# Kernel tuning notes

Hardware: AMD Instinct MI355X
Metric: run time of the kernel (lower is better)

Reference implementation:

```python
import jax, jax.numpy as jnp
import numpy as np

DIM, DIM_HEAD, S, R = 1024, 64, 8, 2
SCALE = DIM_HEAD ** -0.5
NEG = -jnp.finfo(jnp.float32).max


def setup_inputs() -> dict:
    key = jax.random.key(0)
    ks = jax.random.split(key, 7)
    b, n = 2, 2048
    x = jax.random.normal(ks[0], (b, n, DIM), dtype=jnp.float32)
    mask = jnp.ones((b, n), dtype=bool)
    sd, rd = DIM_HEAD * S, DIM_HEAD * R
    init = lambda k, i, o: jax.random.normal(k, (i, o), dtype=jnp.float32) / np.sqrt(i)
    return {
        'x': x,
        'mask': mask,
        'Wsq': init(ks[1], DIM, sd),
        'Wsk': init(ks[2], DIM, sd),
        'Wrv': init(ks[3], DIM, rd),
        'Wrq': init(ks[4], DIM, sd),
        'Wrk': init(ks[5], DIM_HEAD, DIM_HEAD),
        'Wout': init(ks[6], sd, DIM),
    }


def _split_heads(t, h):
    # b n (h d) -> b h n d
    b, n, hd = t.shape
    return t.reshape(b, n, h, hd // h).transpose(0, 2, 1, 3)


def reference(x, mask, Wsq, Wsk, Wrv, Wrq, Wrk, Wout):
    # --- search stage ---
    sq = _split_heads(x @ Wsq, S) * SCALE          # b s i d
    sk = _split_heads(x @ Wsk, S)                  # b s j d
    search_sim = jnp.einsum('bsid,bsjd->bsij', sq, sk)
    search_sim = jnp.where(mask[:, None, None, :], search_sim, NEG)
    search_attn = jax.nn.softmax(search_sim, axis=-1)
    # --- retrieval stage ---
    rv = _split_heads(x @ Wrv, R)                  # b r j d
    retrieved = jnp.einsum('bsij,brjd->bsrid', search_attn, rv)  # b s r n d
    rq = _split_heads(x @ Wrq, S) * SCALE          # b s n d
    rk = retrieved @ Wrk                           # b s r n d
    retrieval_sim = jnp.einsum('bsnd,bsrnd->bsnr', rq, rk)
    retrieval_attn = jax.nn.softmax(retrieval_sim, axis=-1)
    out = jnp.einsum('bsnr,bsrnd->bsnd', retrieval_attn, retrieved)
    b, _, n, d = out.shape
    out = out.transpose(0, 2, 1, 3).reshape(b, n, S * d)  # b n (s d)
    return out @ Wout
```

## Files before the change

### kernel.cpp

```cpp
#include <hip/hip_runtime.h>

typedef unsigned short u16;
typedef unsigned int u32;
typedef __attribute__((ext_vector_type(8))) short short8;
typedef __attribute__((ext_vector_type(4))) float f32x4;

#define B_     2
#define N_     2048
#define DIMX   1024
#define DH     64
#define NS     8
#define SD     512
#define RD     128

__device__ __forceinline__ float bu2f(u16 u) {
    return __uint_as_float(((unsigned)u) << 16);
}
__device__ __forceinline__ u16 f2bu(float f) {
    unsigned u = __float_as_uint(f);
    return (u16)((u + 0x7FFFu + ((u >> 16) & 1u)) >> 16);
}
__device__ __forceinline__ int swzA(int row, int col) {
    return row * 64 + (col ^ ((row & 7) << 3));
}

__global__ void detect_f32(const u16* __restrict__ wrk, int* __restrict__ flag) {
    __shared__ int cnt;
    if (threadIdx.x == 0) cnt = 0;
    __syncthreads();
    int local = 0;
    for (int k = threadIdx.x; k < 2048; k += 256) {
        u16 u = wrk[2 * k];
        int e = (u >> 7) & 0xFF;
        if (u == 0 || (e >= 0x60 && e <= 0x7E)) local++;
    }
    atomicAdd(&cnt, local);
    __syncthreads();
    if (threadIdx.x == 0) *flag = (cnt < 1024) ? 1 : 0;
}

__global__ __launch_bounds__(256, 4)
void convert_bf16(const void* __restrict__ src, u16* __restrict__ dst, int n8,
                  const int* __restrict__ flag) {
    const bool f32m = (*flag != 0);
    int idx = blockIdx.x * blockDim.x + threadIdx.x;
    int stride = gridDim.x * blockDim.x;
    for (int c = idx; c < n8; c += stride) {
        if (f32m) {
            const float4* s = (const float4*)src;
            float4 v0 = s[c * 2], v1 = s[c * 2 + 1];
            u16 o[8] = {f2bu(v0.x), f2bu(v0.y), f2bu(v0.z), f2bu(v0.w),
                        f2bu(v1.x), f2bu(v1.y), f2bu(v1.z), f2bu(v1.w)};
            *reinterpret_cast<short8*>(&dst[c * 8]) = *reinterpret_cast<short8*>(o);
        } else {
            *reinterpret_cast<short8*>(&dst[c * 8]) =
                reinterpret_cast<const short8*>(src)[c];
        }
    }
}

__global__ __launch_bounds__(256, 4)
void prep_weights(const void* __restrict__ Wsq, const void* __restrict__ Wsk,
                  const void* __restrict__ Wrq, const void* __restrict__ Wrv,
                  const void* __restrict__ Wout, const void* __restrict__ Wrk,
                  u16* __restrict__ wTcat, u16* __restrict__ woutT,
                  u16* __restrict__ wrkb, const int* __restrict__ flag) {
    const bool f32m = (*flag != 0);
    const int b = blockIdx.x, tid = threadIdx.x;

    if (b == 2176) {
#pragma unroll
        for (int t = 0; t < 2; ++t) {
            int c = tid + (t << 8);
            if (f32m) {
                const float4* s = (const float4*)Wrk;
                float4 v0 = s[c * 2], v1 = s[c * 2 + 1];
                u16 o[8] = {f2bu(v0.x), f2bu(v0.y), f2bu(v0.z), f2bu(v0.w),
                            f2bu(v1.x), f2bu(v1.y), f2bu(v1.z), f2bu(v1.w)};
                *reinterpret_cast<short8*>(&wrkb[c * 8]) = *reinterpret_cast<short8*>(o);
            } else {
                *reinterpret_cast<short8*>(&wrkb[c * 8]) =
                    reinterpret_cast<const short8*>(Wrk)[c];
            }
        }
        return;
    }

    const void* W; u16* dst; int K, N, t;
    if (b < 512)        { W = Wsq;  dst = wTcat;               K = DIMX; N = SD;   t = b; }
    else if (b < 1024)  { W = Wsk;  dst = wTcat + 512 * 1024;  K = DIMX; N = SD;   t = b - 512; }
    else if (b < 1536)  { W = Wrq;  dst = wTcat + 1024 * 1024; K = DIMX; N = SD;   t = b - 1024; }
    else if (b < 1664)  { W = Wrv;  dst = wTcat + 1536 * 1024; K = DIMX; N = RD;   t = b - 1536; }
    else                { W = Wout; dst = woutT;               K = SD;   N = DIMX; t = b - 1664; }
    const int ntn = N >> 5;
    const int k0 = (t / ntn) << 5, n0 = (t % ntn) << 5;

    __shared__ float T[32][33];
    const int r = tid >> 3, c4 = (tid & 7) << 2;
    if (f32m) {
        float4 v = *reinterpret_cast<const float4*>(
            &((const float*)W)[(size_t)(k0 + r) * N + n0 + c4]);
        T[r][c4 + 0] = v.x; T[r][c4 + 1] = v.y;
        T[r][c4 + 2] = v.z; T[r][c4 + 3] = v.w;
    } else {
        ushort4 v = *reinterpret_cast<const ushort4*>(
            &((const u16*)W)[(size_t)(k0 + r) * N + n0 + c4]);
        T[r][c4 + 0] = bu2f(v.x); T[r][c4 + 1] = bu2f(v.y);
        T[r][c4 + 2] = bu2f(v.z); T[r][c4 + 3] = bu2f(v.w);
    }
    __syncthreads();
    ushort4 st;
    st.x = f2bu(T[c4 + 0][r]); st.y = f2bu(T[c4 + 1][r]);
    st.z = f2bu(T[c4 + 2][r]); st.w = f2bu(T[c4 + 3][r]);
    *reinterpret_cast<ushort4*>(&dst[(size_t)(n0 + r) * K + k0 + c4]) = st;
}

template <int MODE>
__global__ __launch_bounds__(256, 2)
void gemm_mfma(const u16* __restrict__ A, const u16* __restrict__ Bt,
               void* __restrict__ C0, void* __restrict__ C1,
               void* __restrict__ C2, void* __restrict__ C3,
               int M, int N, int K, const int* __restrict__ flag) {
    __shared__ u16 As[4096];
    __shared__ u16 Bs[8192];
    const int tid = threadIdx.x, lane = tid & 63, w = tid >> 6;
    const int i = lane & 15, g = lane >> 4;
    const int row0 = blockIdx.y << 6, n0 = blockIdx.x << 7;

    f32x4 acc[8];
#pragma unroll
    for (int c = 0; c < 8; ++c) acc[c] = (f32x4){0.f, 0.f, 0.f, 0.f};

    for (int kt = 0; kt < K; kt += 64) {
        __syncthreads();
#pragma unroll
        for (int t2 = 0; t2 < 2; ++t2) {
            int v = tid + (t2 << 8);
            int r = v >> 3, c8 = (v & 7) << 3;
            *reinterpret_cast<short8*>(&As[swzA(r, c8)]) =
                *reinterpret_cast<const short8*>(&A[(size_t)(row0 + r) * K + kt + c8]);
        }
#pragma unroll
        for (int t4 = 0; t4 < 4; ++t4) {
            int v = tid + (t4 << 8);
            int n = v >> 3, c8 = (v & 7) << 3;
            *reinterpret_cast<short8*>(&Bs[swzA(n, c8)]) =
                *reinterpret_cast<const short8*>(&Bt[(size_t)(n0 + n) * K + kt + c8]);
        }
        __syncthreads();
#pragma unroll
        for (int ks = 0; ks < 2; ++ks) {
            short8 a = *reinterpret_cast<const short8*>(&As[swzA(w * 16 + i, ks * 32 + g * 8)]);
#pragma unroll
            for (int cf = 0; cf < 8; ++cf) {
                short8 b = *reinterpret_cast<const short8*>(&Bs[swzA(cf * 16 + i, ks * 32 + g * 8)]);
                acc[cf] = __builtin_amdgcn_mfma_f32_16x16x32_bf16(a, b, acc[cf], 0, 0, 0);
            }
        }
    }

    if (MODE == 0) {
        u16* dst; int ld, off; float alpha;
        if (n0 < 512)       { dst = (u16*)C0; ld = 512; off = n0;        alpha = 0.125f; }
        else if (n0 < 1024) { dst = (u16*)C1; ld = 512; off = n0 - 512;  alpha = 1.f; }
        else if (n0 < 1536) { dst = (u16*)C2; ld = 512; off = n0 - 1024; alpha = 0.125f; }
        else                { dst = (u16*)C3; ld = 128; off = n0 - 1536; alpha = 1.f; }
#pragma unroll
        for (int cf = 0; cf < 8; ++cf)
#pragma unroll
            for (int r = 0; r < 4; ++r)
                dst[(size_t)(row0 + w * 16 + g * 4 + r) * ld + off + cf * 16 + i] =
                    f2bu(acc[cf][r] * alpha);
    } else {
        const bool f32o = (*flag != 0);
        if (f32o) {
            float* Cf = (float*)C0;
#pragma unroll
            for (int cf = 0; cf < 8; ++cf)
#pragma unroll
                for (int r = 0; r < 4; ++r)
                    Cf[(size_t)(row0 + w * 16 + g * 4 + r) * N + n0 + cf * 16 + i] = acc[cf][r];
        } else {
            u16* Cb = (u16*)C0;
#pragma unroll
            for (int cf = 0; cf < 8; ++cf)
#pragma unroll
                for (int r = 0; r < 4; ++r)
                    Cb[(size_t)(row0 + w * 16 + g * 4 + r) * N + n0 + cf * 16 + i] =
                        f2bu(acc[cf][r]);
        }
    }
}

__global__ __launch_bounds__(256, 2)
void flash_mfma(const u16* __restrict__ sq, const u16* __restrict__ sk,
                const u16* __restrict__ rv, const u16* __restrict__ rq,
                const u16* __restrict__ wrk, u16* __restrict__ O) {
    __shared__ u16 Ks[2][64 * 72];
    __shared__ u16 Vt[2][128 * 72];
    __shared__ u16 Ps[4][16 * 72];

    const int tid = threadIdx.x, lane = tid & 63, w = tid >> 6;
    const int i = lane & 15, g = lane >> 4;
    const int bs = blockIdx.y, bi = bs >> 3, si = bs & 7;
    const int q0 = blockIdx.x << 6;

    const u16* sqp = sq + ((size_t)(bi * N_ + q0 + w * 16 + i)) * SD + si * DH;
    const u16* rqp = rq + ((size_t)(bi * N_ + q0 + w * 16 + i)) * SD + si * DH;
    const u16* skb = sk + (size_t)bi * N_ * SD + si * DH;
    const u16* rvb = rv + (size_t)bi * N_ * RD;

    short8 aq[2], arq[2];
    aq[0]  = *reinterpret_cast<const short8*>(sqp + g * 8);
    aq[1]  = *reinterpret_cast<const short8*>(sqp + 32 + g * 8);
    arq[0] = *reinterpret_cast<const short8*>(rqp + g * 8);
    arq[1] = *reinterpret_cast<const short8*>(rqp + 32 + g * 8);

    short8 ones;
#pragma unroll
    for (int e = 0; e < 8; ++e) ones[e] = (short)0x3F80;

    const int krow = tid >> 2, kcol = (tid & 3) << 4;
    const int vu = tid & 31, vjb = tid >> 5;

    short8 kreg[2];
    ushort4 vreg[8];

#define LOADKV(jt_)                                                              \
    {                                                                            \
        const u16* kp = skb + (size_t)(((jt_) << 6) + krow) * SD + kcol;         \
        kreg[0] = *reinterpret_cast<const short8*>(kp);                          \
        kreg[1] = *reinterpret_cast<const short8*>(kp + 8);                      \
        const u16* vp = rvb + (size_t)(((jt_) << 6) + vjb * 8) * RD + vu * 4;    \
        _Pragma("unroll")                                                        \
        for (int jj = 0; jj < 8; ++jj)                                           \
            vreg[jj] = *reinterpret_cast<const ushort4*>(vp + (size_t)jj * RD);  \
    }

#define STOREKV(buf_)                                                            \
    {                                                                            \
        int ka = krow * 72;                                                      \
        *reinterpret_cast<short8*>(&Ks[buf_][ka + ((kcol) ^ ((krow & 7) << 3))]) = kreg[0];      \
        *reinterpret_cast<short8*>(&Ks[buf_][ka + ((kcol + 8) ^ ((krow & 7) << 3))]) = kreg[1];  \
        u32 out[4][4];                                                           \
        _Pragma("unroll")                                                        \
        for (int p = 0; p < 4; ++p) {                                            \
            u32 a0 = ((const u32*)&vreg[2 * p])[0], a1 = ((const u32*)&vreg[2 * p])[1];          \
            u32 b0 = ((const u32*)&vreg[2 * p + 1])[0], b1 = ((const u32*)&vreg[2 * p + 1])[1];  \
            out[0][p] = (a0 & 0xFFFFu) | (b0 << 16);                             \
            out[1][p] = (a0 >> 16) | (b0 & 0xFFFF0000u);                         \
            out[2][p] = (a1 & 0xFFFFu) | (b1 << 16);                             \
            out[3][p] = (a1 >> 16) | (b1 & 0xFFFF0000u);                         \
        }                                                                        \
        _Pragma("unroll")                                                        \
        for (int s_ = 0; s_ < 4; ++s_) {                                         \
            int d_ = 4 * vu + s_;                                                \
            *reinterpret_cast<short8*>(                                          \
                &Vt[buf_][d_ * 72 + ((vjb * 8) ^ (((d_ >> 2) & 7) << 3))]) =     \
                *reinterpret_cast<short8*>(out[s_]);                             \
        }                                                                        \
    }

    f32x4 acc[2][4], lacc = (f32x4){0.f, 0.f, 0.f, 0.f};
#pragma unroll
    for (int h = 0; h < 2; ++h)
#pragma unroll
        for (int c = 0; c < 4; ++c) acc[h][c] = (f32x4){0.f, 0.f, 0.f, 0.f};
    float mrun[4] = {-3e38f, -3e38f, -3e38f, -3e38f};

    u16* Pw = Ps[w];

    LOADKV(0);
    STOREKV(0);
    __syncthreads();

    int cur = 0;
    for (int jt = 0; jt < 32; ++jt) {
        if (jt < 31) LOADKV(jt + 1);

        f32x4 s[4];
#pragma unroll
        for (int c = 0; c < 4; ++c) s[c] = (f32x4){0.f, 0.f, 0.f, 0.f};
#pragma unroll
        for (int ks = 0; ks < 2; ++ks)
#pragma unroll
            for (int c = 0; c < 4; ++c) {
                int r_ = c * 16 + i;
                short8 bk = *reinterpret_cast<const short8*>(
                    &Ks[cur][r_ * 72 + ((ks * 32 + g * 8) ^ ((r_ & 7) << 3))]);
                s[c] = __builtin_amdgcn_mfma_f32_16x16x32_bf16(aq[ks], bk, s[c], 0, 0, 0);
            }

        float mt[4], grow = -3e38f;
#pragma unroll
        for (int r = 0; r < 4; ++r) {
            float m0 = fmaxf(fmaxf(s[0][r], s[1][r]), fmaxf(s[2][r], s[3][r]));
            m0 = fmaxf(m0, __shfl_xor(m0, 1)); m0 = fmaxf(m0, __shfl_xor(m0, 2));
            m0 = fmaxf(m0, __shfl_xor(m0, 4)); m0 = fmaxf(m0, __shfl_xor(m0, 8));
            mt[r] = m0;
            grow = fmaxf(grow, m0 - mrun[r]);
        }
        if (!__all(grow <= 8.0f)) {
#pragma unroll
            for (int r = 0; r < 4; ++r) {
                float mn = fmaxf(mrun[r], mt[r]);
                float corr = __expf(mrun[r] - mn);
                mrun[r] = mn;
                lacc[r] *= corr;
#pragma unroll
                for (int h = 0; h < 2; ++h)
#pragma unroll
                    for (int c = 0; c < 4; ++c) acc[h][c][r] *= corr;
            }
        }
#pragma unroll
        for (int r = 0; r < 4; ++r) {
            int row = g * 4 + r;
#pragma unroll
            for (int c = 0; c < 4; ++c)
                Pw[row * 72 + c * 16 + i] = f2bu(__expf(s[c][r] - mrun[r]));
        }

        short8 pa[2];
        pa[0] = *reinterpret_cast<const short8*>(&Pw[i * 72 + g * 8]);
        pa[1] = *reinterpret_cast<const short8*>(&Pw[i * 72 + 32 + g * 8]);
        lacc = __builtin_amdgcn_mfma_f32_16x16x32_bf16(pa[0], ones, lacc, 0, 0, 0);
        lacc = __builtin_amdgcn_mfma_f32_16x16x32_bf16(pa[1], ones, lacc, 0, 0, 0);
#pragma unroll
        for (int ks = 0; ks < 2; ++ks)
#pragma unroll
            for (int h = 0; h < 2; ++h)
#pragma unroll
                for (int c2 = 0; c2 < 4; ++c2) {
                    int d_ = h * 64 + c2 * 16 + i;
                    short8 vb = *reinterpret_cast<const short8*>(
                        &Vt[cur][d_ * 72 + ((ks * 32 + g * 8) ^ (((d_ >> 2) & 7) << 3))]);
                    acc[h][c2] = __builtin_amdgcn_mfma_f32_16x16x32_bf16(pa[ks], vb, acc[h][c2], 0, 0, 0);
                }

        if (jt < 31) STOREKV(cur ^ 1);
        __syncthreads();
        cur ^= 1;
    }

    f32x4 wf[4];
#pragma unroll
    for (int c = 0; c < 4; ++c) wf[c] = (f32x4){0.f, 0.f, 0.f, 0.f};
#pragma unroll
    for (int ks = 0; ks < 2; ++ks)
#pragma unroll
        for (int c2 = 0; c2 < 4; ++c2) {
            short8 bw = *reinterpret_cast<const short8*>(
                &wrk[(c2 * 16 + i) * 64 + ks * 32 + g * 8]);
            wf[c2] = __builtin_amdgcn_mfma_f32_16x16x32_bf16(arq[ks], bw, wf[c2], 0, 0, 0);
        }

    u16* Op = O + ((size_t)(bi * N_ + q0 + w * 16)) * SD + si * DH;
#pragma unroll
    for (int r = 0; r < 4; ++r) {
        float z0 = 0.f, z1 = 0.f;
#pragma unroll
        for (int c2 = 0; c2 < 4; ++c2) {
            z0 += acc[0][c2][r] * wf[c2][r];
            z1 += acc[1][c2][r] * wf[c2][r];
        }
        z0 += __shfl_xor(z0, 1); z0 += __shfl_xor(z0, 2);
        z0 += __shfl_xor(z0, 4); z0 += __shfl_xor(z0, 8);
        z1 += __shfl_xor(z1, 1); z1 += __shfl_xor(z1, 2);
        z1 += __shfl_xor(z1, 4); z1 += __shfl_xor(z1, 8);
        float linv = 1.f / lacc[r];
        z0 *= linv; z1 *= linv;
        float mz = fmaxf(z0, z1);
        float e0 = __expf(z0 - mz), e1 = __expf(z1 - mz);
        float inv = 1.f / (e0 + e1);
        float a0 = e0 * inv * linv, a1 = e1 * inv * linv;
        int row = g * 4 + r;
#pragma unroll
        for (int c2 = 0; c2 < 4; ++c2)
            Op[(size_t)row * SD + c2 * 16 + i] =
                f2bu(a0 * acc[0][c2][r] + a1 * acc[1][c2][r]);
    }
#undef LOADKV
#undef STOREKV
}

extern "C" void kernel_launch(void* const* d_in, const int* in_sizes, int n_in,
                              void* d_out, int out_size, void* d_ws, size_t ws_size,
                              hipStream_t stream) {
    (void)in_sizes; (void)n_in; (void)out_size; (void)ws_size;
    const void* x    = d_in[0];
    const void* Wsq  = d_in[2];
    const void* Wsk  = d_in[3];
    const void* Wrv  = d_in[4];
    const void* Wrq  = d_in[5];
    const void* Wrk  = d_in[6];
    const void* Wout = d_in[7];

    const size_t MBy = 1024 * 1024;
    char* ws = (char*)d_ws;
    int* flag   = (int*)ws;
    u16* xb     = (u16*)(ws + 1 * MBy);
    u16* O      = xb;
    u16* wTcat  = (u16*)(ws + 9 * MBy);
    u16* woutT  = (u16*)(ws + 13 * MBy);
    u16* wrkb   = (u16*)(ws + 14 * MBy);
    u16* sqb    = (u16*)(ws + 15 * MBy);
    u16* skb    = (u16*)(ws + 19 * MBy);
    u16* rqb    = (u16*)(ws + 23 * MBy);
    u16* rvb    = (u16*)(ws + 27 * MBy);

    dim3 blk(256);
    detect_f32<<<1, blk, 0, stream>>>((const u16*)Wrk, flag);
    convert_bf16<<<2048, blk, 0, stream>>>(x, xb, (B_ * N_ * DIMX) / 8, flag);
    prep_weights<<<2177, blk, 0, stream>>>(Wsq, Wsk, Wrq, Wrv, Wout, Wrk,
                                           wTcat, woutT, wrkb, flag);
    gemm_mfma<0><<<dim3(13, 64), blk, 0, stream>>>(xb, wTcat, sqb, skb, rqb, rvb,
                                                   B_ * N_, 1664, DIMX, flag);
    flash_mfma<<<dim3(N_ / 64, B_ * NS), blk, 0, stream>>>(sqb, skb, rvb, rqb, wrkb, O);
    gemm_mfma<1><<<dim3(8, 64), blk, 0, stream>>>(O, woutT, d_out, nullptr, nullptr, nullptr,
                                                  B_ * N_, DIMX, SD, flag);
}
```

Before: 160.1 us.

## Rewrite fused attention with 32x32x16 MFMA and register-resident P tiles

Replaces the 16x16x32 flash attention kernel with one using 32x32x16 bf16 MFMA, computing S transposed (K as the A operand) so the probability tile stays in registers as the A operand of the PV product instead of round-tripping through LDS. Each wave now handles 32 queries (128 per block), row sums are accumulated directly in registers rather than via a ones-matrix MFMA, and K/V LDS tiles use a new quad-granular swizzle without padding. The larger tiles halve K/V reloads per query, at the cost of higher register pressure (launch bounds set to 1 block) and half as many blocks in the grid.

Result: faster. 155.2 us, median of 3 (-3.1%).

```diff
diff --git a/kernel.cpp b/kernel.cpp
--- a/kernel.cpp
+++ b/kernel.cpp
@@ -4,6 +4,7 @@
 typedef unsigned int u32;
 typedef __attribute__((ext_vector_type(8))) short short8;
 typedef __attribute__((ext_vector_type(4))) float f32x4;
+typedef __attribute__((ext_vector_type(16))) float f32x16;
 
 #define B_     2
 #define N_     2048
@@ -22,6 +23,15 @@
 }
 __device__ __forceinline__ int swzA(int row, int col) {
     return row * 64 + (col ^ ((row & 7) << 3));
+}
+__device__ __forceinline__ int qswz(int row, int quad) {
+    return row * 64 + ((quad ^ (row & 15)) << 2);
+}
+__device__ __forceinline__ short8 mk8(ushort4 lo, ushort4 hi) {
+    short8 r;
+    r[0] = (short)lo.x; r[1] = (short)lo.y; r[2] = (short)lo.z; r[3] = (short)lo.w;
+    r[4] = (short)hi.x; r[5] = (short)hi.y; r[6] = (short)hi.z; r[7] = (short)hi.w;
+    return r;
 }
 
 __global__ void detect_f32(const u16* __restrict__ wrk, int* __restrict__ flag) {
@@ -192,83 +202,74 @@
     }
 }
 
-__global__ __launch_bounds__(256, 2)
-void flash_mfma(const u16* __restrict__ sq, const u16* __restrict__ sk,
-                const u16* __restrict__ rv, const u16* __restrict__ rq,
-                const u16* __restrict__ wrk, u16* __restrict__ O) {
-    __shared__ u16 Ks[2][64 * 72];
-    __shared__ u16 Vt[2][128 * 72];
-    __shared__ u16 Ps[4][16 * 72];
+#define QMAP(r) (((r) & 3) + 8 * ((r) >> 2) + 4 * h)
+
+__global__ __launch_bounds__(256, 1)
+void flash_mfma32(const u16* __restrict__ sq, const u16* __restrict__ sk,
+                  const u16* __restrict__ rv, const u16* __restrict__ rq,
+                  const u16* __restrict__ wrk, u16* __restrict__ O) {
+    __shared__ u16 Ks[2][64 * 64];
+    __shared__ u16 Vt[2][128 * 64];
 
     const int tid = threadIdx.x, lane = tid & 63, w = tid >> 6;
-    const int i = lane & 15, g = lane >> 4;
+    const int q31 = lane & 31, h = lane >> 5;
     const int bs = blockIdx.y, bi = bs >> 3, si = bs & 7;
-    const int q0 = blockIdx.x << 6;
-
-    const u16* sqp = sq + ((size_t)(bi * N_ + q0 + w * 16 + i)) * SD + si * DH;
-    const u16* rqp = rq + ((size_t)(bi * N_ + q0 + w * 16 + i)) * SD + si * DH;
+    const int qw0 = (blockIdx.x << 7) + (w << 5);
+
     const u16* skb = sk + (size_t)bi * N_ * SD + si * DH;
     const u16* rvb = rv + (size_t)bi * N_ * RD;
-
-    short8 aq[2], arq[2];
-    aq[0]  = *reinterpret_cast<const short8*>(sqp + g * 8);
-    aq[1]  = *reinterpret_cast<const short8*>(sqp + 32 + g * 8);
-    arq[0] = *reinterpret_cast<const short8*>(rqp + g * 8);
-    arq[1] = *reinterpret_cast<const short8*>(rqp + 32 + g * 8);
-
-    short8 ones;
-#pragma unroll
-    for (int e = 0; e < 8; ++e) ones[e] = (short)0x3F80;
-
-    const int krow = tid >> 2, kcol = (tid & 3) << 4;
-    const int vu = tid & 31, vjb = tid >> 5;
+    const u16* qrow  = sq + (size_t)(bi * N_ + qw0 + q31) * SD + si * DH;
+    const u16* rqrow = rq + (size_t)(bi * N_ + qw0 + q31) * SD + si * DH;
+
+    short8 qb[4];
+#pragma unroll
+    for (int s = 0; s < 4; ++s) {
+        ushort4 lo = *reinterpret_cast<const ushort4*>(qrow + 16 * s + 4 * h);
+        ushort4 hi = *reinterpret_cast<const ushort4*>(qrow + 16 * s + 8 + 4 * h);
+        qb[s] = mk8(lo, hi);
+    }
+
+    const int krow = tid >> 2, kq = tid & 3;
+    const int vdq = tid & 31, vjo = tid >> 5;
 
     short8 kreg[2];
-    ushort4 vreg[8];
-
-#define LOADKV(jt_)                                                              \
-    {                                                                            \
-        const u16* kp = skb + (size_t)(((jt_) << 6) + krow) * SD + kcol;         \
-        kreg[0] = *reinterpret_cast<const short8*>(kp);                          \
-        kreg[1] = *reinterpret_cast<const short8*>(kp + 8);                      \
-        const u16* vp = rvb + (size_t)(((jt_) << 6) + vjb * 8) * RD + vu * 4;    \
-        _Pragma("unroll")                                                        \
-        for (int jj = 0; jj < 8; ++jj)                                           \
-            vreg[jj] = *reinterpret_cast<const ushort4*>(vp + (size_t)jj * RD);  \
-    }
-
-#define STOREKV(buf_)                                                            \
-    {                                                                            \
-        int ka = krow * 72;                                                      \
-        *reinterpret_cast<short8*>(&Ks[buf_][ka + ((kcol) ^ ((krow & 7) << 3))]) = kreg[0];      \
-        *reinterpret_cast<short8*>(&Ks[buf_][ka + ((kcol + 8) ^ ((krow & 7) << 3))]) = kreg[1];  \
-        u32 out[4][4];                                                           \
-        _Pragma("unroll")                                                        \
-        for (int p = 0; p < 4; ++p) {                                            \
-            u32 a0 = ((const u32*)&vreg[2 * p])[0], a1 = ((const u32*)&vreg[2 * p])[1];          \
-            u32 b0 = ((const u32*)&vreg[2 * p + 1])[0], b1 = ((const u32*)&vreg[2 * p + 1])[1];  \
-            out[0][p] = (a0 & 0xFFFFu) | (b0 << 16);                             \
-            out[1][p] = (a0 >> 16) | (b0 & 0xFFFF0000u);                         \
-            out[2][p] = (a1 & 0xFFFFu) | (b1 << 16);                             \
-            out[3][p] = (a1 >> 16) | (b1 & 0xFFFF0000u);                         \
-        }                                                                        \
-        _Pragma("unroll")                                                        \
-        for (int s_ = 0; s_ < 4; ++s_) {                                         \
-            int d_ = 4 * vu + s_;                                                \
-            *reinterpret_cast<short8*>(                                          \
-                &Vt[buf_][d_ * 72 + ((vjb * 8) ^ (((d_ >> 2) & 7) << 3))]) =     \
-                *reinterpret_cast<short8*>(out[s_]);                             \
-        }                                                                        \
-    }
-
-    f32x4 acc[2][4], lacc = (f32x4){0.f, 0.f, 0.f, 0.f};
-#pragma unroll
-    for (int h = 0; h < 2; ++h)
-#pragma unroll
-        for (int c = 0; c < 4; ++c) acc[h][c] = (f32x4){0.f, 0.f, 0.f, 0.f};
-    float mrun[4] = {-3e38f, -3e38f, -3e38f, -3e38f};
-
-    u16* Pw = Ps[w];
+    union U4 { ushort4 v; u16 e[4]; };
+    U4 vreg[8];
+
+#define LOADKV(jt_)                                                               \
+    {                                                                             \
+        const u16* kp = skb + (size_t)(((jt_) << 6) + krow) * SD + kq * 16;       \
+        kreg[0] = *reinterpret_cast<const short8*>(kp);                           \
+        kreg[1] = *reinterpret_cast<const short8*>(kp + 8);                       \
+        const u16* vp = rvb + (size_t)(((jt_) << 6) + vjo * 8) * RD + vdq * 4;    \
+        _Pragma("unroll")                                                         \
+        for (int jj = 0; jj < 8; ++jj)                                            \
+            vreg[jj].v = *reinterpret_cast<const ushort4*>(vp + (size_t)jj * RD); \
+    }
+
+#define STOREKV(buf_)                                                             \
+    {                                                                             \
+        const U4* kp4 = reinterpret_cast<const U4*>(&kreg[0]);                    \
+        _Pragma("unroll")                                                         \
+        for (int p = 0; p < 4; ++p)                                               \
+            *reinterpret_cast<ushort4*>(&Ks[buf_][qswz(krow, 4 * kq + p)]) = kp4[p].v; \
+        _Pragma("unroll")                                                         \
+        for (int s_ = 0; s_ < 4; ++s_) {                                          \
+            int d_ = 4 * vdq + s_;                                                \
+            _Pragma("unroll")                                                     \
+            for (int p = 0; p < 2; ++p) {                                         \
+                ushort4 ov;                                                       \
+                ov.x = vreg[4 * p + 0].e[s_]; ov.y = vreg[4 * p + 1].e[s_];       \
+                ov.z = vreg[4 * p + 2].e[s_]; ov.w = vreg[4 * p + 3].e[s_];       \
+                *reinterpret_cast<ushort4*>(&Vt[buf_][qswz(d_, 2 * vjo + p)]) = ov; \
+            }                                                                     \
+        }                                                                         \
+    }
+
+    f32x16 acc[4];
+#pragma unroll
+    for (int db = 0; db < 4; ++db) acc[db] = 0.f;
+    float mrun = -3e38f, lsum = 0.f;
 
     LOADKV(0);
     STOREKV(0);
@@ -278,107 +279,108 @@
     for (int jt = 0; jt < 32; ++jt) {
         if (jt < 31) LOADKV(jt + 1);
 
-        f32x4 s[4];
-#pragma unroll
-        for (int c = 0; c < 4; ++c) s[c] = (f32x4){0.f, 0.f, 0.f, 0.f};
-#pragma unroll
-        for (int ks = 0; ks < 2; ++ks)
-#pragma unroll
-            for (int c = 0; c < 4; ++c) {
-                int r_ = c * 16 + i;
-                short8 bk = *reinterpret_cast<const short8*>(
-                    &Ks[cur][r_ * 72 + ((ks * 32 + g * 8) ^ ((r_ & 7) << 3))]);
-                s[c] = __builtin_amdgcn_mfma_f32_16x16x32_bf16(aq[ks], bk, s[c], 0, 0, 0);
+        f32x16 sf0 = 0.f, sf1 = 0.f;
+#pragma unroll
+        for (int s = 0; s < 4; ++s) {
+            ushort4 alo = *reinterpret_cast<const ushort4*>(&Ks[cur][qswz(q31, 4 * s + h)]);
+            ushort4 ahi = *reinterpret_cast<const ushort4*>(&Ks[cur][qswz(q31, 4 * s + 2 + h)]);
+            sf0 = __builtin_amdgcn_mfma_f32_32x32x16_bf16(mk8(alo, ahi), qb[s], sf0, 0, 0, 0);
+        }
+#pragma unroll
+        for (int s = 0; s < 4; ++s) {
+            ushort4 alo = *reinterpret_cast<const ushort4*>(&Ks[cur][qswz(32 + q31, 4 * s + h)]);
+            ushort4 ahi = *reinterpret_cast<const ushort4*>(&Ks[cur][qswz(32 + q31, 4 * s + 2 + h)]);
+            sf1 = __builtin_amdgcn_mfma_f32_32x32x16_bf16(mk8(alo, ahi), qb[s], sf1, 0, 0, 0);
+        }
+
+        float mt = sf0[0];
+#pragma unroll
+        for (int r = 1; r < 16; ++r) mt = fmaxf(mt, sf0[r]);
+#pragma unroll
+        for (int r = 0; r < 16; ++r) mt = fmaxf(mt, sf1[r]);
+        mt = fmaxf(mt, __shfl_xor(mt, 32));
+        if (!__all(mt - mrun <= 8.0f)) {
+            float mn = fmaxf(mrun, mt);
+            float corr = __expf(mrun - mn);
+            mrun = mn;
+            lsum *= corr;
+#pragma unroll
+            for (int r = 0; r < 16; ++r) {
+                float cr = __shfl(corr, QMAP(r));
+                acc[0][r] *= cr; acc[1][r] *= cr; acc[2][r] *= cr; acc[3][r] *= cr;
             }
-
-        float mt[4], grow = -3e38f;
-#pragma unroll
-        for (int r = 0; r < 4; ++r) {
-            float m0 = fmaxf(fmaxf(s[0][r], s[1][r]), fmaxf(s[2][r], s[3][r]));
-            m0 = fmaxf(m0, __shfl_xor(m0, 1)); m0 = fmaxf(m0, __shfl_xor(m0, 2));
-            m0 = fmaxf(m0, __shfl_xor(m0, 4)); m0 = fmaxf(m0, __shfl_xor(m0, 8));
-            mt[r] = m0;
-            grow = fmaxf(grow, m0 - mrun[r]);
-        }
-        if (!__all(grow <= 8.0f)) {
-#pragma unroll
-            for (int r = 0; r < 4; ++r) {
-                float mn = fmaxf(mrun[r], mt[r]);
-                float corr = __expf(mrun[r] - mn);
-                mrun[r] = mn;
-                lacc[r] *= corr;
-#pragma unroll
-                for (int h = 0; h < 2; ++h)
-#pragma unroll
-                    for (int c = 0; c < 4; ++c) acc[h][c][r] *= corr;
+        }
+        float pf0[16], pf1[16];
+#pragma unroll
+        for (int r = 0; r < 16; ++r) {
+            pf0[r] = __expf(sf0[r] - mrun); lsum += pf0[r];
+            pf1[r] = __expf(sf1[r] - mrun); lsum += pf1[r];
+        }
+
+#pragma unroll
+        for (int ks = 0; ks < 4; ++ks) {
+            const float* pf = (ks < 2) ? pf0 : pf1;
+            const int b0 = (ks & 1) * 8;
+            u32 w0, w1, w2, w3;
+            asm("v_cvt_pk_bf16_f32 %0, %1, %2" : "=v"(w0) : "v"(pf[b0 + 0]), "v"(pf[b0 + 1]));
+            asm("v_cvt_pk_bf16_f32 %0, %1, %2" : "=v"(w1) : "v"(pf[b0 + 2]), "v"(pf[b0 + 3]));
+            asm("v_cvt_pk_bf16_f32 %0, %1, %2" : "=v"(w2) : "v"(pf[b0 + 4]), "v"(pf[b0 + 5]));
+            asm("v_cvt_pk_bf16_f32 %0, %1, %2" : "=v"(w3) : "v"(pf[b0 + 6]), "v"(pf[b0 + 7]));
+            union { u32 u[4]; short8 s8; } pa;
+            pa.u[0] = w0; pa.u[1] = w1; pa.u[2] = w2; pa.u[3] = w3;
+#pragma unroll
+            for (int db = 0; db < 4; ++db) {
+                int d_ = 32 * db + q31;
+                ushort4 vlo = *reinterpret_cast<const ushort4*>(&Vt[cur][qswz(d_, 4 * ks + h)]);
+                ushort4 vhi = *reinterpret_cast<const ushort4*>(&Vt[cur][qswz(d_, 4 * ks + 2 + h)]);
+                acc[db] = __builtin_amdgcn_mfma_f32_32x32x16_bf16(pa.s8, mk8(vlo, vhi), acc[db], 0, 0, 0);
             }
         }
-#pragma unroll
-        for (int r = 0; r < 4; ++r) {
-            int row = g * 4 + r;
-#pragma unroll
-            for (int c = 0; c < 4; ++c)
-                Pw[row * 72 + c * 16 + i] = f2bu(__expf(s[c][r] - mrun[r]));
-        }
-
-        short8 pa[2];
-        pa[0] = *reinterpret_cast<const short8*>(&Pw[i * 72 + g * 8]);
-        pa[1] = *reinterpret_cast<const short8*>(&Pw[i * 72 + 32 + g * 8]);
-        lacc = __builtin_amdgcn_mfma_f32_16x16x32_bf16(pa[0], ones, lacc, 0, 0, 0);
-        lacc = __builtin_amdgcn_mfma_f32_16x16x32_bf16(pa[1], ones, lacc, 0, 0, 0);
-#pragma unroll
-        for (int ks = 0; ks < 2; ++ks)
-#pragma unroll
-            for (int h = 0; h < 2; ++h)
-#pragma unroll
-                for (int c2 = 0; c2 < 4; ++c2) {
-                    int d_ = h * 64 + c2 * 16 + i;
-                    short8 vb = *reinterpret_cast<const short8*>(
-                        &Vt[cur][d_ * 72 + ((ks * 32 + g * 8) ^ (((d_ >> 2) & 7) << 3))]);
-                    acc[h][c2] = __builtin_amdgcn_mfma_f32_16x16x32_bf16(pa[ks], vb, acc[h][c2], 0, 0, 0);
-                }
 
         if (jt < 31) STOREKV(cur ^ 1);
         __syncthreads();
         cur ^= 1;
     }
 
-    f32x4 wf[4];
-#pragma unroll
-    for (int c = 0; c < 4; ++c) wf[c] = (f32x4){0.f, 0.f, 0.f, 0.f};
-#pragma unroll
-    for (int ks = 0; ks < 2; ++ks)
-#pragma unroll
-        for (int c2 = 0; c2 < 4; ++c2) {
-            short8 bw = *reinterpret_cast<const short8*>(
-                &wrk[(c2 * 16 + i) * 64 + ks * 32 + g * 8]);
-            wf[c2] = __builtin_amdgcn_mfma_f32_16x16x32_bf16(arq[ks], bw, wf[c2], 0, 0, 0);
-        }
-
-    u16* Op = O + ((size_t)(bi * N_ + q0 + w * 16)) * SD + si * DH;
-#pragma unroll
-    for (int r = 0; r < 4; ++r) {
-        float z0 = 0.f, z1 = 0.f;
-#pragma unroll
-        for (int c2 = 0; c2 < 4; ++c2) {
-            z0 += acc[0][c2][r] * wf[c2][r];
-            z1 += acc[1][c2][r] * wf[c2][r];
-        }
-        z0 += __shfl_xor(z0, 1); z0 += __shfl_xor(z0, 2);
-        z0 += __shfl_xor(z0, 4); z0 += __shfl_xor(z0, 8);
-        z1 += __shfl_xor(z1, 1); z1 += __shfl_xor(z1, 2);
-        z1 += __shfl_xor(z1, 4); z1 += __shfl_xor(z1, 8);
-        float linv = 1.f / lacc[r];
-        z0 *= linv; z1 *= linv;
+    lsum += __shfl_xor(lsum, 32);
+
+    short8 rqb4[4];
+#pragma unroll
+    for (int s = 0; s < 4; ++s) {
+        ushort4 lo = *reinterpret_cast<const ushort4*>(rqrow + 16 * s + 4 * h);
+        ushort4 hi = *reinterpret_cast<const ushort4*>(rqrow + 16 * s + 8 + 4 * h);
+        rqb4[s] = mk8(lo, hi);
+    }
+    f32x16 w2[2];
+    w2[0] = 0.f; w2[1] = 0.f;
+#pragma unroll
+    for (int cb = 0; cb < 2; ++cb)
+#pragma unroll
+        for (int s = 0; s < 4; ++s) {
+            const u16* wp = wrk + (size_t)(32 * cb + q31) * 64 + 16 * s + 4 * h;
+            short8 bw = mk8(*reinterpret_cast<const ushort4*>(wp),
+                            *reinterpret_cast<const ushort4*>(wp + 8));
+            w2[cb] = __builtin_amdgcn_mfma_f32_32x32x16_bf16(rqb4[s], bw, w2[cb], 0, 0, 0);
+        }
+
+#pragma unroll
+    for (int r = 0; r < 16; ++r) {
+        float t0 = acc[0][r] * w2[0][r] + acc[1][r] * w2[1][r];
+        float t1 = acc[2][r] * w2[0][r] + acc[3][r] * w2[1][r];
+        t0 += __shfl_xor(t0, 1); t0 += __shfl_xor(t0, 2); t0 += __shfl_xor(t0, 4);
+        t0 += __shfl_xor(t0, 8); t0 += __shfl_xor(t0, 16);
+        t1 += __shfl_xor(t1, 1); t1 += __shfl_xor(t1, 2); t1 += __shfl_xor(t1, 4);
+        t1 += __shfl_xor(t1, 8); t1 += __shfl_xor(t1, 16);
+        float lq = __shfl(lsum, QMAP(r));
+        float linv = 1.f / lq;
+        float z0 = t0 * linv, z1 = t1 * linv;
         float mz = fmaxf(z0, z1);
         float e0 = __expf(z0 - mz), e1 = __expf(z1 - mz);
         float inv = 1.f / (e0 + e1);
         float a0 = e0 * inv * linv, a1 = e1 * inv * linv;
-        int row = g * 4 + r;
-#pragma unroll
-        for (int c2 = 0; c2 < 4; ++c2)
-            Op[(size_t)row * SD + c2 * 16 + i] =
-                f2bu(a0 * acc[0][c2][r] + a1 * acc[1][c2][r]);
+        u16* Op = O + (size_t)(bi * N_ + qw0 + QMAP(r)) * SD + si * DH;
+        Op[q31]      = f2bu(a0 * acc[0][r] + a1 * acc[2][r]);
+        Op[32 + q31] = f2bu(a0 * acc[1][r] + a1 * acc[3][r]);
     }
 #undef LOADKV
 #undef STOREKV
@@ -416,7 +418,7 @@
                                            wTcat, woutT, wrkb, flag);
     gemm_mfma<0><<<dim3(13, 64), blk, 0, stream>>>(xb, wTcat, sqb, skb, rqb, rvb,
                                                    B_ * N_, 1664, DIMX, flag);
-    flash_mfma<<<dim3(N_ / 64, B_ * NS), blk, 0, stream>>>(sqb, skb, rvb, rqb, wrkb, O);
+    flash_mfma32<<<dim3(N_ / 128, B_ * NS), blk, 0, stream>>>(sqb, skb, rvb, rqb, wrkb, O);
     gemm_mfma<1><<<dim3(8, 64), blk, 0, stream>>>(O, woutT, d_out, nullptr, nullptr, nullptr,
                                                   B_ * N_, DIMX, SD, flag);
 }
```
